# Kernel tuning notes

Measured on AMD Instinct MI355X. Metric: run time of the kernel, lower is better.

Reference implementation:

```python
import jax, jax.numpy as jnp
import numpy as np


def setup_inputs() -> dict:
    key = jax.random.key(0)
    ks = jax.random.split(key, 6)
    N, T, D, H = 256, 128, 512, 512
    x = jax.random.normal(ks[0], (N, T, D), dtype=jnp.float32)
    A = jax.random.normal(ks[1], (N, H, 4, 4), dtype=jnp.float32)
    Wx = jax.random.normal(ks[2], (D, 4 * H), dtype=jnp.float32) / np.sqrt(D)
    Wh = jax.random.normal(ks[3], (H, 4 * H), dtype=jnp.float32) / np.sqrt(H)
    Wattn = jax.random.normal(ks[4], (H, 4 * H), dtype=jnp.float32) / np.sqrt(H)
    b = jnp.zeros((4 * H,), dtype=jnp.float32)
    return {"x": x, "A": A, "Wx": Wx, "Wh": Wh, "Wattn": Wattn, "b": b}


def reference(x, A, Wx, Wh, Wattn, b):
    N, T, D = x.shape
    H = Wh.shape[0]
    A_flat = A.reshape(N, H, -1)  # (N, H, 16)
    h0 = A_flat.mean(axis=-1)     # mean over 4x4 grid
    c0 = h0
    inv_sqrt_H = 1.0 / np.sqrt(H).astype(np.float32)

    def step(carry, x_t):
        h, c = carry
        # scaled dot-product attention over the 16 spatial cells
        scores = jnp.einsum('nh,nhp->np', h, A_flat) * inv_sqrt_H  # (N, 16)
        w = jax.nn.softmax(scores, axis=-1)
        attn = jnp.einsum('nhp,np->nh', A_flat, w)                 # (N, H)
        a = x_t @ Wx + h @ Wh + attn @ Wattn + b                   # (N, 4H)
        a_i, a_f, a_o, a_g = jnp.split(a, 4, axis=1)
        i = jax.nn.sigmoid(a_i)
        f = jax.nn.sigmoid(a_f)
        o = jax.nn.sigmoid(a_o)
        g = jnp.tanh(a_g)
        c_next = f * c + i * g
        h_next = o * jnp.tanh(c_next)
        return (h_next, c_next), h_next

    _, hs = jax.lax.scan(step, (h0, c0), jnp.swapaxes(x, 0, 1))  # (T, N, H)
    return jnp.swapaxes(hs, 0, 1)  # (N, T, H)
```

## Files before the change

### kernel.cpp

```cpp
#include <hip/hip_runtime.h>
#include <math.h>

typedef unsigned short u16;
typedef _Float16 h16;
typedef _Float16 f16x8 __attribute__((ext_vector_type(8)));
typedef float f32x4 __attribute__((ext_vector_type(4)));

__device__ __forceinline__ float sigm(float x) { return 1.f / (1.f + expf(-x)); }


__global__ void k_pack_w(const float* __restrict__ Wx, const float* __restrict__ Wh,
                         const float* __restrict__ Wat,
                         h16* __restrict__ WhiS, h16* __restrict__ WloS) {
  unsigned idx = blockIdx.x * 256 + threadIdx.x;
  unsigned e = idx & 7, l = (idx >> 3) & 63, cf = (idx >> 9) & 1;
  unsigned t2 = idx >> 10;
  unsigned j = t2 / 48u, ks = t2 - j * 48u;
  unsigned k = ks * 32 + ((l >> 4) << 3) + e;
  unsigned c32 = cf * 16 + (l & 15);
  unsigned acol = (c32 >> 3) * 512 + j * 8 + (c32 & 7);
  float v = (k < 512) ? Wx[(size_t)k * 2048 + acol]
          : (k < 1024) ? Wh[(size_t)(k - 512) * 2048 + acol]
                       : Wat[(size_t)(k - 1024) * 2048 + acol];
  h16 hi = (h16)v;
  WhiS[idx] = hi;
  WloS[idx] = (h16)((v - (float)hi) * 4096.f);
}

__global__ void k_xsplit(const float* __restrict__ x, h16* __restrict__ xhi,
                         h16* __restrict__ xlo) {
  size_t i = ((size_t)blockIdx.x * 256 + threadIdx.x) * 4;
  float4 v = *(const float4*)(x + i);
  union { h16 h[4]; uint2 u; } a, b;
  float vv[4] = {v.x, v.y, v.z, v.w};
#pragma unroll
  for (int e = 0; e < 4; ++e) {
    h16 hh = (h16)vv[e];
    a.h[e] = hh;
    b.h[e] = (h16)((vv[e] - (float)hh) * 4096.f);
  }
  *(uint2*)(xhi + i) = a.u;
  *(uint2*)(xlo + i) = b.u;
}

__global__ void k_init(const float* __restrict__ Af, float* __restrict__ h32,
                       h16* __restrict__ hhi, h16* __restrict__ hlo,
                       float* __restrict__ cst) {
  int idx = blockIdx.x * 256 + threadIdx.x;
  const float* ap = Af + (size_t)idx * 16;
  float s = 0.f;
#pragma unroll
  for (int p = 0; p < 16; ++p) s += ap[p];
  s *= 0.0625f;
  h32[idx] = s;
  cst[idx] = s;
  h16 hh = (h16)s;
  hhi[idx] = hh;
  hlo[idx] = (h16)((s - (float)hh) * 4096.f);
}

__global__ __launch_bounds__(512) void k_phaseA(const float* __restrict__ Af,
                                                const float* __restrict__ h32,
                                                h16* __restrict__ ahiB,
                                                h16* __restrict__ aloB, int t) {
  __shared__ float SC[8192];
  __shared__ float ared[512];
  __shared__ float wlds[16];
  const int tid = threadIdx.x;
  const int n = blockIdx.x;

  float Areg[16];
  const f32x4* A4 = (const f32x4*)(Af + (size_t)n * 8192 + tid * 16);
#pragma unroll
  for (int q4 = 0; q4 < 4; ++q4) {
    f32x4 v = A4[q4];
#pragma unroll
    for (int e = 0; e < 4; ++e) Areg[q4 * 4 + e] = v[e];
  }
  float hk = h32[(size_t)(t & 1) * 131072 + (size_t)n * 512 + tid];
#pragma unroll
  for (int p = 0; p < 16; ++p) SC[tid * 16 + p] = hk * Areg[p];
  __syncthreads();
  {
    int seg = tid >> 4, pp = tid & 15;
    float s = 0.f;
#pragma unroll
    for (int q = 0; q < 16; ++q) s += SC[(seg * 16 + q) * 16 + pp];
    ared[seg * 16 + pp] = s;
  }
  __syncthreads();
  if (tid < 16) {
    float s = 0.f;
#pragma unroll
    for (int q = 0; q < 32; ++q) s += ared[q * 16 + tid];
    s *= 0.04419417382415922f;
    float m = s;
#pragma unroll
    for (int o = 8; o >= 1; o >>= 1) m = fmaxf(m, __shfl_xor(m, o, 16));
    float e = __expf(s - m);
    float se = e;
#pragma unroll
    for (int o = 8; o >= 1; o >>= 1) se += __shfl_xor(se, o, 16);
    wlds[tid] = e / se;
  }
  __syncthreads();
  float av = 0.f;
#pragma unroll
  for (int p = 0; p < 16; ++p) av += Areg[p] * wlds[p];
  h16 ah = (h16)av;
  ahiB[(size_t)n * 512 + tid] = ah;
  aloB[(size_t)n * 512 + tid] = (h16)((av - (float)ah) * 4096.f);
}

template<bool XPRE>
__global__ __launch_bounds__(512, 4) void k_gemm(
    const float* __restrict__ bv,
    const float* __restrict__ x, const h16* __restrict__ xhi, const h16* __restrict__ xlo,
    const h16* __restrict__ WhiS, const h16* __restrict__ WloS,
    float* __restrict__ h32, h16* __restrict__ hhi, h16* __restrict__ hlo,
    const h16* __restrict__ ahiB, const h16* __restrict__ aloB,
    float* __restrict__ cst, float* __restrict__ out, int t) {
  __shared__ float P[7 * 1056];

  const int tid = threadIdx.x;
  const int l = tid & 63, wv = tid >> 6;
  const int bid = blockIdx.x;
  const int g = bid >> 6;
  const int j = (bid & 7) * 8 + ((bid >> 3) & 7);
  const int n0 = g * 32;
  const int rA = n0 + (l & 15);
  const int klane = (l >> 4) * 8;

  const h16* whiJ = WhiS + (size_t)j * 49152;
  const h16* wloJ = WloS + (size_t)j * 49152;

  const int rC = tid >> 3, qC = tid & 7;
  const int colC = j * 8 + qC;
  const float b_i = bv[colC], b_f = bv[512 + colC], b_o = bv[1024 + colC],
              b_g = bv[1536 + colC];

  const int rb = t & 1, wb = rb ^ 1;
  const h16* hhiR = hhi + (size_t)rb * 131072;
  const h16* hloR = hlo + (size_t)rb * 131072;

  f32x4 acc1[2][2], acc2[2][2];
#pragma unroll
  for (int rt = 0; rt < 2; ++rt)
#pragma unroll
    for (int cf = 0; cf < 2; ++cf) {
      acc1[rt][cf] = (f32x4){0.f, 0.f, 0.f, 0.f};
      acc2[rt][cf] = (f32x4){0.f, 0.f, 0.f, 0.f};
    }

  auto kstep = [&](int ksg) {
    const f16x8 bh0 = *(const f16x8*)(whiJ + ((size_t)(ksg * 2 + 0) * 64 + l) * 8);
    const f16x8 bh1 = *(const f16x8*)(whiJ + ((size_t)(ksg * 2 + 1) * 64 + l) * 8);
    const f16x8 bl0 = *(const f16x8*)(wloJ + ((size_t)(ksg * 2 + 0) * 64 + l) * 8);
    const f16x8 bl1 = *(const f16x8*)(wloJ + ((size_t)(ksg * 2 + 1) * 64 + l) * 8);
    f16x8 Ah[2], Al[2];
    const int kg = ksg * 32;
    if (kg < 512) {
      const size_t base = ((size_t)rA * 128 + t) * 512 + kg + klane;
      if (XPRE) {
#pragma unroll
        for (int rt = 0; rt < 2; ++rt) {
          Ah[rt] = *(const f16x8*)(xhi + base + (size_t)rt * 1048576);
          Al[rt] = *(const f16x8*)(xlo + base + (size_t)rt * 1048576);
        }
      } else {
#pragma unroll
        for (int rt = 0; rt < 2; ++rt) {
          const float* xp = x + base + (size_t)rt * 1048576;
          f32x4 v0 = *(const f32x4*)xp, v1 = *(const f32x4*)(xp + 4);
          float vv[8] = {v0[0], v0[1], v0[2], v0[3], v1[0], v1[1], v1[2], v1[3]};
#pragma unroll
          for (int e = 0; e < 8; ++e) {
            h16 hh = (h16)vv[e];
            Ah[rt][e] = hh;
            Al[rt][e] = (h16)((vv[e] - (float)hh) * 4096.f);
          }
        }
      }
    } else if (kg < 1024) {
      const size_t base = (size_t)rA * 512 + (kg - 512) + klane;
#pragma unroll
      for (int rt = 0; rt < 2; ++rt) {
        Ah[rt] = *(const f16x8*)(hhiR + base + rt * 8192);
        Al[rt] = *(const f16x8*)(hloR + base + rt * 8192);
      }
    } else {
      const size_t base = (size_t)rA * 512 + (kg - 1024) + klane;
#pragma unroll
      for (int rt = 0; rt < 2; ++rt) {
        Ah[rt] = *(const f16x8*)(ahiB + base + rt * 8192);
        Al[rt] = *(const f16x8*)(aloB + base + rt * 8192);
      }
    }
#pragma unroll
    for (int rt = 0; rt < 2; ++rt) {
      acc1[rt][0] = __builtin_amdgcn_mfma_f32_16x16x32_f16(Ah[rt], bh0, acc1[rt][0], 0, 0, 0);
      acc1[rt][1] = __builtin_amdgcn_mfma_f32_16x16x32_f16(Ah[rt], bh1, acc1[rt][1], 0, 0, 0);
      acc2[rt][0] = __builtin_amdgcn_mfma_f32_16x16x32_f16(Al[rt], bh0, acc2[rt][0], 0, 0, 0);
      acc2[rt][1] = __builtin_amdgcn_mfma_f32_16x16x32_f16(Al[rt], bh1, acc2[rt][1], 0, 0, 0);
      acc2[rt][0] = __builtin_amdgcn_mfma_f32_16x16x32_f16(Ah[rt], bl0, acc2[rt][0], 0, 0, 0);
      acc2[rt][1] = __builtin_amdgcn_mfma_f32_16x16x32_f16(Ah[rt], bl1, acc2[rt][1], 0, 0, 0);
    }
  };

#pragma unroll
  for (int i = 0; i < 6; ++i) kstep(wv + 8 * i);

  float accf[2][2][4];
#pragma unroll
  for (int rt = 0; rt < 2; ++rt)
#pragma unroll
    for (int cf = 0; cf < 2; ++cf)
#pragma unroll
      for (int rg = 0; rg < 4; ++rg)
        accf[rt][cf][rg] = acc1[rt][cf][rg] + acc2[rt][cf][rg] * (1.f / 4096.f);

  auto publish = [&](int slot) {
#pragma unroll
    for (int rt = 0; rt < 2; ++rt)
#pragma unroll
      for (int cf = 0; cf < 2; ++cf)
#pragma unroll
        for (int rg = 0; rg < 4; ++rg)
          P[slot * 1056 + (rt * 16 + (l >> 4) * 4 + rg) * 33 + cf * 16 + (l & 15)] =
              accf[rt][cf][rg];
  };
  auto addin = [&](int slot) {
#pragma unroll
    for (int rt = 0; rt < 2; ++rt)
#pragma unroll
      for (int cf = 0; cf < 2; ++cf)
#pragma unroll
        for (int rg = 0; rg < 4; ++rg)
          accf[rt][cf][rg] +=
              P[slot * 1056 + (rt * 16 + (l >> 4) * 4 + rg) * 33 + cf * 16 + (l & 15)];
  };

  if (wv >= 4) publish(wv - 4);
  __syncthreads();
  if (wv < 4) addin(wv);
  if (wv == 2) publish(4);
  if (wv == 3) publish(5);
  __syncthreads();
  if (wv == 0) addin(4);
  if (wv == 1) { addin(5); publish(6); }
  __syncthreads();
  if (wv == 0) { addin(6); publish(0); }
  __syncthreads();

  if (tid < 256) {
    float ai = P[rC * 33 + qC] + b_i;
    float af_ = P[rC * 33 + 8 + qC] + b_f;
    float ao = P[rC * 33 + 16 + qC] + b_o;
    float ag = P[rC * 33 + 24 + qC] + b_g;
    float ig = sigm(ai), fg = sigm(af_), og = sigm(ao), gg = tanhf(ag);
    const size_t cix = (size_t)(n0 + rC) * 512 + colC;
    float c = cst[cix];
    float cn = fg * c + ig * gg;
    cst[cix] = cn;
    float hn = og * tanhf(cn);
    h32[(size_t)wb * 131072 + cix] = hn;
    h16 hh = (h16)hn;
    hhi[(size_t)wb * 131072 + cix] = hh;
    hlo[(size_t)wb * 131072 + cix] = (h16)((hn - (float)hh) * 4096.f);
    out[((size_t)(n0 + rC) * 128 + t) * 512 + colC] = hn;
  }
}


extern "C" void kernel_launch(void* const* d_in, const int* in_sizes, int n_in,
                              void* d_out, int out_size, void* d_ws, size_t ws_size,
                              hipStream_t stream) {
  (void)in_sizes; (void)n_in; (void)out_size;
  const float* x   = (const float*)d_in[0];
  const float* Af  = (const float*)d_in[1];
  const float* Wx  = (const float*)d_in[2];
  const float* Wh  = (const float*)d_in[3];
  const float* Wat = (const float*)d_in[4];
  const float* bv  = (const float*)d_in[5];
  float* out = (float*)d_out;

  char* ws = (char*)d_ws;
  size_t off = 0;
  auto alloc = [&](size_t nb) {
    char* p = ws + off; off = (off + nb + 255) & ~(size_t)255; return p;
  };
  h16*   WhiS = (h16*)alloc(3145728ull * 2);
  h16*   WloS = (h16*)alloc(3145728ull * 2);
  float* h32  = (float*)alloc(262144ull * 4);
  h16*   hhi  = (h16*)alloc(262144ull * 2);
  h16*   hlo  = (h16*)alloc(262144ull * 2);
  h16*   ahiB = (h16*)alloc(131072ull * 2);
  h16*   aloB = (h16*)alloc(131072ull * 2);
  float* cst  = (float*)alloc(131072ull * 4);
  size_t base_end = off;
  h16* xhi = (h16*)alloc(16777216ull * 2);
  h16* xlo = (h16*)alloc(16777216ull * 2);
  bool xpre = (ws_size >= base_end + 2ull * 16777216ull * 2 + 4096);

  k_pack_w<<<12288, 256, 0, stream>>>(Wx, Wh, Wat, WhiS, WloS);
  k_init<<<512, 256, 0, stream>>>(Af, h32, hhi, hlo, cst);
  if (xpre) k_xsplit<<<16384, 256, 0, stream>>>(x, xhi, xlo);

  for (int t = 0; t < 128; ++t) {
    k_phaseA<<<256, 512, 0, stream>>>(Af, h32, ahiB, aloB, t);
    if (xpre)
      k_gemm<true><<<512, 512, 0, stream>>>(bv, x, xhi, xlo, WhiS, WloS,
                                            h32, hhi, hlo, ahiB, aloB, cst, out, t);
    else
      k_gemm<false><<<512, 512, 0, stream>>>(bv, x, xhi, xlo, WhiS, WloS,
                                             h32, hhi, hlo, ahiB, aloB, cst, out, t);
  }
}
```

Baseline: 2.769 ms.

## Precompute per-sample attention-weight products to drop attention GEMM slice

Reassociates attn@Wattn as a softmax-weighted sum of precomputed per-sample matrices A[n,:,p]@Wattn, computed once in double precision. The per-step GEMM K dimension shrinks from 1536 to 1024, and phaseA now only emits 16 softmax weights per sample. In exchange each step streams a large 32 MB precomputed tensor in the gate epilogue, and a heavy FP64 precompute kernel is added.

```diff
diff --git a/kernel.cpp b/kernel.cpp
--- a/kernel.cpp
+++ b/kernel.cpp
@@ -10,21 +10,50 @@
 
 
 __global__ void k_pack_w(const float* __restrict__ Wx, const float* __restrict__ Wh,
-                         const float* __restrict__ Wat,
                          h16* __restrict__ WhiS, h16* __restrict__ WloS) {
   unsigned idx = blockIdx.x * 256 + threadIdx.x;
   unsigned e = idx & 7, l = (idx >> 3) & 63, cf = (idx >> 9) & 1;
   unsigned t2 = idx >> 10;
-  unsigned j = t2 / 48u, ks = t2 - j * 48u;
+  unsigned j = t2 >> 5, ks = t2 & 31;
   unsigned k = ks * 32 + ((l >> 4) << 3) + e;
   unsigned c32 = cf * 16 + (l & 15);
   unsigned acol = (c32 >> 3) * 512 + j * 8 + (c32 & 7);
   float v = (k < 512) ? Wx[(size_t)k * 2048 + acol]
-          : (k < 1024) ? Wh[(size_t)(k - 512) * 2048 + acol]
-                       : Wat[(size_t)(k - 1024) * 2048 + acol];
+                      : Wh[(size_t)(k - 512) * 2048 + acol];
   h16 hi = (h16)v;
   WhiS[idx] = hi;
   WloS[idx] = (h16)((v - (float)hi) * 4096.f);
+}
+
+__global__ __launch_bounds__(256) void k_m(const float* __restrict__ Af,
+                                           const float* __restrict__ Wat,
+                                           float* __restrict__ M2) {
+  __shared__ float Alds[8192];
+  const int tid = threadIdx.x;
+  const int cb = blockIdx.x;
+  const int n  = blockIdx.y;
+  {
+    const float4* src = (const float4*)(Af + (size_t)n * 8192);
+    float4* dst = (float4*)Alds;
+    for (int i = tid; i < 2048; i += 256) dst[i] = src[i];
+  }
+  __syncthreads();
+  const int c0 = cb * 512 + tid * 2;
+  double acc0[16], acc1[16];
+#pragma unroll
+  for (int p = 0; p < 16; ++p) { acc0[p] = 0.0; acc1[p] = 0.0; }
+  for (int k = 0; k < 512; ++k) {
+    float2 wv2 = *(const float2*)(Wat + (size_t)k * 2048 + c0);
+    const float* ar = Alds + k * 16;
+#pragma unroll
+    for (int p = 0; p < 16; ++p) {
+      acc0[p] += (double)ar[p] * (double)wv2.x;
+      acc1[p] += (double)ar[p] * (double)wv2.y;
+    }
+  }
+  float* o = M2 + ((size_t)n * 2048 + c0) * 16;
+#pragma unroll
+  for (int p = 0; p < 16; ++p) { o[p] = (float)acc0[p]; o[16 + p] = (float)acc1[p]; }
 }
 
 __global__ void k_xsplit(const float* __restrict__ x, h16* __restrict__ xhi,
@@ -61,11 +90,9 @@
 
 __global__ __launch_bounds__(512) void k_phaseA(const float* __restrict__ Af,
                                                 const float* __restrict__ h32,
-                                                h16* __restrict__ ahiB,
-                                                h16* __restrict__ aloB, int t) {
+                                                float* __restrict__ wbuf, int t) {
   __shared__ float SC[8192];
   __shared__ float ared[512];
-  __shared__ float wlds[16];
   const int tid = threadIdx.x;
   const int n = blockIdx.x;
 
@@ -101,15 +128,8 @@
     float se = e;
 #pragma unroll
     for (int o = 8; o >= 1; o >>= 1) se += __shfl_xor(se, o, 16);
-    wlds[tid] = e / se;
-  }
-  __syncthreads();
-  float av = 0.f;
-#pragma unroll
-  for (int p = 0; p < 16; ++p) av += Areg[p] * wlds[p];
-  h16 ah = (h16)av;
-  ahiB[(size_t)n * 512 + tid] = ah;
-  aloB[(size_t)n * 512 + tid] = (h16)((av - (float)ah) * 4096.f);
+    wbuf[n * 16 + tid] = e / se;
+  }
 }
 
 template<bool XPRE>
@@ -117,10 +137,11 @@
     const float* __restrict__ bv,
     const float* __restrict__ x, const h16* __restrict__ xhi, const h16* __restrict__ xlo,
     const h16* __restrict__ WhiS, const h16* __restrict__ WloS,
+    const float* __restrict__ Mws, const float* __restrict__ wbuf,
     float* __restrict__ h32, h16* __restrict__ hhi, h16* __restrict__ hlo,
-    const h16* __restrict__ ahiB, const h16* __restrict__ aloB,
     float* __restrict__ cst, float* __restrict__ out, int t) {
   __shared__ float P[7 * 1056];
+  __shared__ float wsh[32][17];
 
   const int tid = threadIdx.x;
   const int l = tid & 63, wv = tid >> 6;
@@ -131,8 +152,10 @@
   const int rA = n0 + (l & 15);
   const int klane = (l >> 4) * 8;
 
-  const h16* whiJ = WhiS + (size_t)j * 49152;
-  const h16* wloJ = WloS + (size_t)j * 49152;
+  { int r = tid >> 4, p = tid & 15; wsh[r][p] = wbuf[(n0 + r) * 16 + p]; }
+
+  const h16* whiJ = WhiS + (size_t)j * 32768;
+  const h16* wloJ = WloS + (size_t)j * 32768;
 
   const int rC = tid >> 3, qC = tid & 7;
   const int colC = j * 8 + qC;
@@ -181,19 +204,12 @@
           }
         }
       }
-    } else if (kg < 1024) {
+    } else {
       const size_t base = (size_t)rA * 512 + (kg - 512) + klane;
 #pragma unroll
       for (int rt = 0; rt < 2; ++rt) {
         Ah[rt] = *(const f16x8*)(hhiR + base + rt * 8192);
         Al[rt] = *(const f16x8*)(hloR + base + rt * 8192);
-      }
-    } else {
-      const size_t base = (size_t)rA * 512 + (kg - 1024) + klane;
-#pragma unroll
-      for (int rt = 0; rt < 2; ++rt) {
-        Ah[rt] = *(const f16x8*)(ahiB + base + rt * 8192);
-        Al[rt] = *(const f16x8*)(aloB + base + rt * 8192);
       }
     }
 #pragma unroll
@@ -208,7 +224,7 @@
   };
 
 #pragma unroll
-  for (int i = 0; i < 6; ++i) kstep(wv + 8 * i);
+  for (int i = 0; i < 4; ++i) kstep(wv + 8 * i);
 
   float accf[2][2][4];
 #pragma unroll
@@ -253,10 +269,20 @@
   __syncthreads();
 
   if (tid < 256) {
-    float ai = P[rC * 33 + qC] + b_i;
-    float af_ = P[rC * 33 + 8 + qC] + b_f;
-    float ao = P[rC * 33 + 16 + qC] + b_o;
-    float ag = P[rC * 33 + 24 + qC] + b_g;
+    const float* Mr = Mws + ((size_t)(n0 + rC) * 2048 + colC) * 16;
+    float am[4];
+#pragma unroll
+    for (int f = 0; f < 4; ++f) {
+      const float* mp = Mr + (size_t)f * 8192;
+      float s = 0.f;
+#pragma unroll
+      for (int p = 0; p < 16; ++p) s += wsh[rC][p] * mp[p];
+      am[f] = s;
+    }
+    float ai = P[rC * 33 + qC] + am[0] + b_i;
+    float af_ = P[rC * 33 + 8 + qC] + am[1] + b_f;
+    float ao = P[rC * 33 + 16 + qC] + am[2] + b_o;
+    float ag = P[rC * 33 + 24 + qC] + am[3] + b_g;
     float ig = sigm(ai), fg = sigm(af_), og = sigm(ao), gg = tanhf(ag);
     const size_t cix = (size_t)(n0 + rC) * 512 + colC;
     float c = cst[cix];
@@ -289,30 +315,31 @@
   auto alloc = [&](size_t nb) {
     char* p = ws + off; off = (off + nb + 255) & ~(size_t)255; return p;
   };
-  h16*   WhiS = (h16*)alloc(3145728ull * 2);
-  h16*   WloS = (h16*)alloc(3145728ull * 2);
+  h16*   WhiS = (h16*)alloc(2097152ull * 2);
+  h16*   WloS = (h16*)alloc(2097152ull * 2);
+  float* Mws  = (float*)alloc(8388608ull * 4);
+  float* wbuf = (float*)alloc(4096ull * 4);
   float* h32  = (float*)alloc(262144ull * 4);
   h16*   hhi  = (h16*)alloc(262144ull * 2);
   h16*   hlo  = (h16*)alloc(262144ull * 2);
-  h16*   ahiB = (h16*)alloc(131072ull * 2);
-  h16*   aloB = (h16*)alloc(131072ull * 2);
   float* cst  = (float*)alloc(131072ull * 4);
   size_t base_end = off;
   h16* xhi = (h16*)alloc(16777216ull * 2);
   h16* xlo = (h16*)alloc(16777216ull * 2);
   bool xpre = (ws_size >= base_end + 2ull * 16777216ull * 2 + 4096);
 
-  k_pack_w<<<12288, 256, 0, stream>>>(Wx, Wh, Wat, WhiS, WloS);
+  k_pack_w<<<8192, 256, 0, stream>>>(Wx, Wh, WhiS, WloS);
+  k_m<<<dim3(4, 256), 256, 0, stream>>>(Af, Wat, Mws);
   k_init<<<512, 256, 0, stream>>>(Af, h32, hhi, hlo, cst);
   if (xpre) k_xsplit<<<16384, 256, 0, stream>>>(x, xhi, xlo);
 
   for (int t = 0; t < 128; ++t) {
-    k_phaseA<<<256, 512, 0, stream>>>(Af, h32, ahiB, aloB, t);
+    k_phaseA<<<256, 512, 0, stream>>>(Af, h32, wbuf, t);
     if (xpre)
-      k_gemm<true><<<512, 512, 0, stream>>>(bv, x, xhi, xlo, WhiS, WloS,
-                                            h32, hhi, hlo, ahiB, aloB, cst, out, t);
+      k_gemm<true><<<512, 512, 0, stream>>>(bv, x, xhi, xlo, WhiS, WloS, Mws, wbuf,
+                                            h32, hhi, hlo, cst, out, t);
     else
-      k_gemm<false><<<512, 512, 0, stream>>>(bv, x, xhi, xlo, WhiS, WloS,
-                                             h32, hhi, hlo, ahiB, aloB, cst, out, t);
-  }
-}
+      k_gemm<false><<<512, 512, 0, stream>>>(bv, x, xhi, xlo, WhiS, WloS, Mws, wbuf,
+                                             h32, hhi, hlo, cst, out, t);
+  }
+}
```

Result: slower. 2.864 ms (+3.4%).
